# Optimization experiments

Hardware: AMD Instinct MI355X
Metric: run time of the kernel (lower is better)

The kernel has to match this reference:

```python
import jax, jax.numpy as jnp
import numpy as np

DIM = 2240; HEADS = 20; HD = 112
B = 1; F = 8; H = 16; W = 28; S = F * H * W; ENC = 300
HID = int(3.0 * DIM)  # 6720
EPS_LN = 1e-6; EPS_RMS = 1e-5


def setup_inputs():
    ks = iter(jax.random.split(jax.random.key(0), 64))
    nrm = lambda shape, s=1.0: jax.random.normal(next(ks), shape, jnp.float32) * s
    wsc = 0.02
    inp = dict(
        hidden_states=nrm((B, S, DIM)),
        encoder_hidden_states=nrm((B, ENC, DIM)),
        timestep=nrm((B, 6 * DIM), 0.1),
        freqs_cos=nrm((1, S, 1, HD)),
        freqs_sin=nrm((1, S, 1, HD)),
        scale_shift_table=nrm((6, DIM), 1.0 / np.sqrt(DIM)),
    )
    for p in ("a1", "a2"):
        inp[p + "_qw"] = nrm((DIM, DIM), wsc); inp[p + "_qb"] = jnp.zeros((DIM,), jnp.float32)
        inp[p + "_kw"] = nrm((DIM, DIM), wsc); inp[p + "_kb"] = jnp.zeros((DIM,), jnp.float32)
        inp[p + "_vw"] = nrm((DIM, DIM), wsc); inp[p + "_vb"] = jnp.zeros((DIM,), jnp.float32)
        inp[p + "_nq"] = jnp.ones((DIM,), jnp.float32)
        inp[p + "_nk"] = jnp.ones((DIM,), jnp.float32)
        inp[p + "_ow"] = nrm((DIM, DIM), wsc); inp[p + "_ob"] = jnp.zeros((DIM,), jnp.float32)
    inp["ff_inv_w"] = nrm((1, 1, DIM, 2 * HID), wsc)
    inp["ff_inv_b"] = jnp.zeros((2 * HID,), jnp.float32)
    inp["ff_depth_w"] = nrm((3, 3, 1, 2 * HID), wsc)
    inp["ff_depth_b"] = jnp.zeros((2 * HID,), jnp.float32)
    inp["ff_point_w"] = nrm((1, 1, HID, DIM), wsc)
    inp["ff_temp_w"] = nrm((3, 1, DIM, DIM), wsc)
    inp["frames"] = F; inp["height"] = H; inp["width"] = W
    return inp


def _ln(x):  # LayerNorm, no affine (elementwise_affine=False)
    m = jnp.mean(x, -1, keepdims=True)
    v = jnp.mean((x - m) ** 2, -1, keepdims=True)
    return (x - m) * jax.lax.rsqrt(v + EPS_LN)


def _rms(x, w):  # rms_norm_across_heads on full inner dim
    return x * jax.lax.rsqrt(jnp.mean(x * x, -1, keepdims=True) + EPS_RMS) * w


def _rope(x, cos, sin):  # interleaved rotary as in SanaLinearAttnProcessor3_0
    x1, x2 = x[..., 0::2], x[..., 1::2]
    c, s = cos[..., 0::2], sin[..., 1::2]
    out = jnp.stack([x1 * c - x2 * s, x1 * s + x2 * c], axis=-1)
    return out.reshape(x.shape)


def _conv(x, k, padding, groups=1):
    return jax.lax.conv_general_dilated(
        x, k, (1, 1), padding,
        dimension_numbers=("NHWC", "HWIO", "NHWC"),
        feature_group_count=groups)


def _linear_attn(x, qw, qb, kw, kb, vw, vb, nq, nk, ow, ob, cos, sin):
    b, s, _ = x.shape
    q = jax.nn.relu(_rms(x @ qw + qb, nq)).reshape(b, s, HEADS, HD)
    k = jax.nn.relu(_rms(x @ kw + kb, nk)).reshape(b, s, HEADS, HD)
    v = (x @ vw + vb).reshape(b, s, HEADS, HD)
    qr, kr = _rope(q, cos, sin), _rope(k, cos, sin)
    ksum = jnp.sum(k, axis=1)                             # [b,h,d] (un-rotated)
    denom = jnp.einsum("bhd,bshd->bsh", ksum, q) + 1e-15  # z^{-1}
    scores = jnp.einsum("bshe,bshd->bhed", v, kr)         # [b,h,dv,d]
    out = jnp.einsum("bhed,bshd->bshe", scores, qr) / denom[..., None]
    return out.reshape(b, s, HEADS * HD) @ ow + ob


def _cross_attn(x, enc, qw, qb, kw, kb, vw, vb, nq, nk, ow, ob):
    b, s, _ = x.shape; t = enc.shape[1]
    q = _rms(x @ qw + qb, nq).reshape(b, s, HEADS, HD)
    k = _rms(enc @ kw + kb, nk).reshape(b, t, HEADS, HD)
    v = (enc @ vw + vb).reshape(b, t, HEADS, HD)
    logits = jnp.einsum("bshd,bthd->bhst", q, k) / np.sqrt(HD).astype(np.float32)
    attn = jax.nn.softmax(logits, axis=-1)
    out = jnp.einsum("bhst,bthd->bshd", attn, v).reshape(b, s, HEADS * HD)
    return out @ ow + ob


def _ff(x, inv_w, inv_b, depth_w, depth_b, point_w, temp_w, f, h, w):
    b = x.shape[0]
    y = x.reshape(b * f, h, w, DIM)
    y = jax.nn.silu(_conv(y, inv_w, "SAME") + inv_b)
    y = _conv(y, depth_w, "SAME", groups=2 * HID) + depth_b
    a, g = y[..., :HID], y[..., HID:]
    y = _conv(a * jax.nn.silu(g), point_w, "SAME")        # [bf,h,w,DIM]
    yt = y.reshape(b, f, h * w, DIM)                      # conv over frames axis
    yt = yt + _conv(yt, temp_w, ((1, 1), (0, 0)))
    return yt.reshape(b, f, h, w, DIM)


def reference(hidden_states, encoder_hidden_states, timestep, freqs_cos, freqs_sin,
              scale_shift_table,
              a1_qw, a1_qb, a1_kw, a1_kb, a1_vw, a1_vb, a1_nq, a1_nk, a1_ow, a1_ob,
              a2_qw, a2_qb, a2_kw, a2_kb, a2_vw, a2_vb, a2_nq, a2_nk, a2_ow, a2_ob,
              ff_inv_w, ff_inv_b, ff_depth_w, ff_depth_b, ff_point_w, ff_temp_w,
              frames, height, width):
    b = hidden_states.shape[0]
    mods = scale_shift_table[None] + timestep.reshape(b, 6, DIM)
    sh_msa, sc_msa, g_msa, sh_mlp, sc_mlp, g_mlp = jnp.split(mods, 6, axis=1)
    nh = _ln(hidden_states) * (1 + sc_msa) + sh_msa
    attn = _linear_attn(nh, a1_qw, a1_qb, a1_kw, a1_kb, a1_vw, a1_vb,
                        a1_nq, a1_nk, a1_ow, a1_ob, freqs_cos, freqs_sin)
    x = hidden_states + g_msa * attn
    x = x + _cross_attn(x, encoder_hidden_states, a2_qw, a2_qb, a2_kw, a2_kb,
                        a2_vw, a2_vb, a2_nq, a2_nk, a2_ow, a2_ob)
    nh = _ln(x) * (1 + sc_mlp) + sh_mlp
    ff = _ff(nh.reshape(b, frames, height, width, DIM),
             ff_inv_w, ff_inv_b, ff_depth_w, ff_depth_b, ff_point_w, ff_temp_w,
             frames, height, width)
    x = x + g_mlp * ff.reshape(b, frames * height * width, DIM)
    return x
```

## Files before the change

kernel.cpp:

```cpp
#include <hip/hip_runtime.h>

#define DIMC 2240
#define STOK 3584
#define ENCT 300
#define NH   20
#define HDIM 112
#define HID1 6720
#define HID2 13440
#define DD   (2240*2240)
#define SD   (3584*2240)

typedef short bf16x8 __attribute__((ext_vector_type(8)));
typedef float f32x4  __attribute__((ext_vector_type(4)));

__device__ __forceinline__ unsigned short f2bf(float f){
  unsigned int u = __float_as_uint(f);
  u += 0x7fffu + ((u >> 16) & 1u);
  return (unsigned short)(u >> 16);
}
__device__ __forceinline__ float bf2f(unsigned short h){
  return __uint_as_float(((unsigned int)h) << 16);
}
__device__ __forceinline__ void gl_lds16(const unsigned short* g, unsigned short* l){
  __builtin_amdgcn_global_load_lds(
      (const __attribute__((address_space(1))) unsigned int*)(const void*)g,
      (__attribute__((address_space(3))) unsigned int*)(void*)l, 16, 0, 0);
}

__global__ void cvt_k(const float4* __restrict__ src, ushort4* __restrict__ dst, int n4){
  int i = blockIdx.x*256 + threadIdx.x;
  if (i < n4){
    float4 v = src[i];
    ushort4 o; o.x = f2bf(v.x); o.y = f2bf(v.y); o.z = f2bf(v.z); o.w = f2bf(v.w);
    dst[i] = o;
  }
}

__global__ __launch_bounds__(256) void cvt_t_k(const float* __restrict__ src,
    unsigned short* __restrict__ dst, int rows, int ldsrc, int c0, int nc){
  __shared__ float tile[32][33];
  const int tx = threadIdx.x & 31, ty = threadIdx.x >> 5;
  const int colBase = blockIdx.x*32;
  #pragma unroll
  for (int i = 0; i < 4; ++i){
    int rr = blockIdx.y*32 + ty + i*8;
    int cc = colBase + tx;
    tile[ty + i*8][tx] = (cc < nc) ? src[(size_t)rr*ldsrc + c0 + cc] : 0.f;
  }
  __syncthreads();
  #pragma unroll
  for (int i = 0; i < 4; ++i){
    int n = colBase + ty + i*8;
    int k = blockIdx.y*32 + tx;
    dst[(size_t)n*rows + k] = f2bf(tile[tx][ty + i*8]);
  }
}

__global__ void pack3_k(float* __restrict__ dst, const float* __restrict__ b0,
    const float* __restrict__ b1, const float* __restrict__ b2, int nslots){
  int i = blockIdx.x*256 + threadIdx.x;
  if (i >= nslots*2304) return;
  int slot = i / 2304, d = i - slot*2304;
  const float* src = (slot == 0) ? b0 : ((slot == 1) ? b1 : b2);
  dst[i] = (d < 2240) ? src[d] : 0.f;
}

__global__ void mods_k(const float* __restrict__ sst, const float* __restrict__ ts, float* __restrict__ mods){
  int i = blockIdx.x*256 + threadIdx.x;
  if (i < 6*DIMC) mods[i] = sst[i] + ts[i];
}

__global__ __launch_bounds__(256) void ln_mod_k(const float* __restrict__ x,
    const float* __restrict__ mods, int shj, int scj, unsigned short* __restrict__ out)
{
  const int s = blockIdx.x;
  const float* row = x + (size_t)s*DIMC;
  const float* sh = mods + shj*DIMC;
  const float* sc = mods + scj*DIMC;
  float sum = 0.f, sq = 0.f;
  for (int d = threadIdx.x; d < DIMC; d += 256){ float v = row[d]; sum += v; sq += v*v; }
  #pragma unroll
  for (int o = 32; o; o >>= 1){ sum += __shfl_down(sum, o); sq += __shfl_down(sq, o); }
  __shared__ float sA[4], sB[4];
  int w = threadIdx.x >> 6, l = threadIdx.x & 63;
  if (!l){ sA[w] = sum; sB[w] = sq; }
  __syncthreads();
  sum = sA[0]+sA[1]+sA[2]+sA[3];
  sq  = sB[0]+sB[1]+sB[2]+sB[3];
  float mean = sum * (1.f/DIMC);
  float rs = rsqrtf(sq*(1.f/DIMC) - mean*mean + 1e-6f);
  unsigned short* orow = out + (size_t)s*DIMC;
  for (int d = threadIdx.x; d < DIMC; d += 256){
    float v = (row[d]-mean)*rs*(1.f + sc[d]) + sh[d];
    orow[d] = f2bf(v);
  }
}

template<int RELU, int ROPE>
__global__ __launch_bounds__(256) void rms_bf_k(unsigned short* __restrict__ x, const float* __restrict__ nw,
    const float* __restrict__ cosb, const float* __restrict__ sinb, unsigned short* __restrict__ xr)
{
  const int s = blockIdx.x;
  unsigned short* row = x + (size_t)s*DIMC;
  float sq = 0.f;
  for (int d = threadIdx.x; d < DIMC; d += 256){ float v = bf2f(row[d]); sq += v*v; }
  #pragma unroll
  for (int o = 32; o; o >>= 1) sq += __shfl_down(sq, o);
  __shared__ float sB[4];
  int w = threadIdx.x >> 6, l = threadIdx.x & 63;
  if (!l) sB[w] = sq;
  __syncthreads();
  sq = sB[0]+sB[1]+sB[2]+sB[3];
  float rs = rsqrtf(sq*(1.f/DIMC) + 1e-5f);
  if constexpr (!ROPE){
    for (int d = threadIdx.x; d < DIMC; d += 256){
      float v = bf2f(row[d])*rs*nw[d];
      if (RELU) v = fmaxf(v, 0.f);
      row[d] = f2bf(v);
    }
  } else {
    for (int p = threadIdx.x; p < DIMC/2; p += 256){
      int d0 = 2*p, d1 = d0+1;
      float v0 = bf2f(row[d0])*rs*nw[d0];
      float v1 = bf2f(row[d1])*rs*nw[d1];
      if (RELU){ v0 = fmaxf(v0,0.f); v1 = fmaxf(v1,0.f); }
      row[d0] = f2bf(v0); row[d1] = f2bf(v1);
      int j0 = d0 % HDIM;
      float c  = cosb[(size_t)s*HDIM + j0];
      float sn = sinb[(size_t)s*HDIM + j0 + 1];
      xr[(size_t)s*DIMC + d0] = f2bf(v0*c - v1*sn);
      xr[(size_t)s*DIMC + d1] = f2bf(v0*sn + v1*c);
    }
  }
}

template<int EPI>
__global__ __launch_bounds__(256) void gemm_bt(
  const unsigned short* __restrict__ A, const unsigned short* __restrict__ Bt,
  const float* __restrict__ bias, float* __restrict__ Cf, unsigned short* __restrict__ Cb,
  const float* __restrict__ res, const float* __restrict__ gate,
  int M, int N, int K, int ldc, int PW)
{
  __shared__ __align__(16) unsigned short Al[128*64];
  __shared__ __align__(16) unsigned short Bl[128*64];
  const int gx = gridDim.x, gy = gridDim.y;
  const int nwg = gx*gy;
  const int orig = blockIdx.y*gx + blockIdx.x;
  const int qq = nwg >> 3, rr = nwg & 7;
  const int xcd = orig & 7, li = orig >> 3;
  const int wg = (xcd < rr ? xcd*(qq+1) : rr*(qq+1) + (xcd-rr)*qq) + li;
  const int ppw = gy*PW;
  const int panel = wg / ppw, rm = wg - panel*ppw;
  const int mrow = rm / PW;
  const int m0 = mrow*128;
  const int n0 = (panel*PW + (rm - mrow*PW))*128;

  const int t = threadIdx.x, lane = t & 63, w = t >> 6;
  const int wr = w >> 1, wc = w & 1;
  const int l16 = lane & 15, lk = lane >> 4;

  const int lr8 = lane >> 3;
  const int sc  = (lane & 7) ^ lr8;
  const unsigned short* Aps[4];
  const unsigned short* Bps[4];
  #pragma unroll
  for (int i = 0; i < 4; ++i){
    int ar = m0 + w*32 + i*8 + lr8;
    int br = n0 + w*32 + i*8 + lr8;
    Aps[i] = A  + (size_t)min(ar, M-1)*K + sc*8;
    Bps[i] = Bt + (size_t)br*K + sc*8;
  }
  unsigned short* Ad = Al + w*2048;
  unsigned short* Bd = Bl + w*2048;

  f32x4 acc[4][4] = {};
  for (int k0 = 0; k0 < K; k0 += 64){
    __syncthreads();
    #pragma unroll
    for (int i = 0; i < 4; ++i){
      gl_lds16(Aps[i] + k0, Ad + i*512);
      gl_lds16(Bps[i] + k0, Bd + i*512);
    }
    __syncthreads();
    #pragma unroll
    for (int kk = 0; kk < 2; ++kk){
      bf16x8 af[4], bfr[4];
      const int chb = (kk*4 + lk) ^ (l16 & 7);
      #pragma unroll
      for (int m = 0; m < 4; ++m)
        af[m] = *reinterpret_cast<const bf16x8*>(Al + (wr*64 + m*16 + l16)*64 + chb*8);
      #pragma unroll
      for (int n = 0; n < 4; ++n)
        bfr[n] = *reinterpret_cast<const bf16x8*>(Bl + (wc*64 + n*16 + l16)*64 + chb*8);
      #pragma unroll
      for (int m = 0; m < 4; ++m)
        #pragma unroll
        for (int n = 0; n < 4; ++n)
          acc[m][n] = __builtin_amdgcn_mfma_f32_16x16x32_bf16(af[m], bfr[n], acc[m][n], 0, 0, 0);
    }
  }

  const int rb = m0 + wr*64 + lk*4;
  const int cb = n0 + wc*64 + l16;
  #pragma unroll
  for (int m = 0; m < 4; ++m){
    #pragma unroll
    for (int r = 0; r < 4; ++r){
      int row = rb + m*16 + r;
      if (row >= M) continue;
      #pragma unroll
      for (int n = 0; n < 4; ++n){
        int col = cb + n*16;
        if (col >= N) continue;
        float v = acc[m][n][r];
        float bv = bias ? bias[col] : 0.f;
        if constexpr (EPI == 6){
          int slot = col / 2304;
          int d = col - slot*2304;
          if (d < 2240)
            Cb[(size_t)slot*ldc + (size_t)row*2240 + d] = f2bf(v + bv);
        } else {
          size_t idx = (size_t)row*ldc + col;
          if constexpr (EPI == 0){ Cf[idx] = v + bv; }
          else if constexpr (EPI == 1){ float u = v + bv; Cb[idx] = f2bf(u / (1.f + __expf(-u))); }
          else if constexpr (EPI == 2){ Cb[idx] = f2bf(v + bv); }
          else if constexpr (EPI == 3){ float u = res[idx] + gate[col]*(v + bv); Cf[idx] = u; Cb[idx] = f2bf(u); }
          else if constexpr (EPI == 4){ Cf[idx] = res[idx] + v + bv; }
          else { Cf[idx] += v; }
        }
      }
    }
  }
}

__global__ void colsum_k(const unsigned short* __restrict__ k, float* __restrict__ kpart){
  int d = blockIdx.x*256 + threadIdx.x;
  if (d >= DIMC) return;
  int ch = blockIdx.y, s0 = ch*128;
  float acc = 0.f;
  for (int s = s0; s < s0+128; ++s) acc += bf2f(k[(size_t)s*DIMC + d]);
  kpart[(size_t)ch*DIMC + d] = acc;
}
__global__ void ksumred_k(const float* __restrict__ kpart, float* __restrict__ ksum){
  int d = blockIdx.x*256 + threadIdx.x;
  if (d >= DIMC) return;
  float a = 0.f;
  for (int c = 0; c < 28; ++c) a += kpart[(size_t)c*DIMC + d];
  ksum[d] = a;
}
__global__ __launch_bounds__(256) void denom_k(const unsigned short* __restrict__ q,
    const float* __restrict__ ksum, float* __restrict__ denom)
{
  int s = blockIdx.x; int w = threadIdx.x >> 6, l = threadIdx.x & 63;
  for (int h = w; h < NH; h += 4){
    const unsigned short* qb = q + (size_t)s*DIMC + h*HDIM;
    const float* kb = ksum + h*HDIM;
    float v = bf2f(qb[l])*kb[l];
    if (l < 48) v += bf2f(qb[64+l])*kb[64+l];
    #pragma unroll
    for (int o = 32; o; o >>= 1) v += __shfl_down(v, o);
    if (!l) denom[s*NH + h] = v + 1e-15f;
  }
}

#define SLSC 136
__device__ __forceinline__ int sc_idx(int e, int s){
  return e*SLSC + (s ^ (((e >> 3) & 7) << 3));
}
__global__ __launch_bounds__(256) void scores_k(const unsigned short* __restrict__ v,
    const unsigned short* __restrict__ kr, float* __restrict__ part)
{
  const int h = blockIdx.x, ch = blockIdx.y;
  __shared__ __align__(16) unsigned short Vt[112*SLSC];
  __shared__ __align__(16) unsigned short Kt[112*SLSC];
  const int t = threadIdx.x, lane = t & 63, w = t >> 6;
  const int l16 = lane & 15, lk = lane >> 4;
  const int sbase = ch*128;

  for (int p = t; p < 1792; p += 256){
    int s = p / 14, oc = (p % 14) * 8;
    bf16x8 vv = *reinterpret_cast<const bf16x8*>(v  + (size_t)(sbase+s)*DIMC + h*HDIM + oc);
    bf16x8 kk = *reinterpret_cast<const bf16x8*>(kr + (size_t)(sbase+s)*DIMC + h*HDIM + oc);
    #pragma unroll
    for (int j = 0; j < 8; ++j){
      Vt[sc_idx(oc+j, s)] = (unsigned short)vv[j];
      Kt[sc_idx(oc+j, s)] = (unsigned short)kk[j];
    }
  }
  __syncthreads();

  f32x4 acc[2][7] = {};
  #pragma unroll
  for (int ks = 0; ks < 4; ++ks){
    const int sf = ks*32 + lk*8;
    bf16x8 bfrg[7];
    #pragma unroll
    for (int nt = 0; nt < 7; ++nt){
      int d = nt*16 + l16;
      bfrg[nt] = *reinterpret_cast<const bf16x8*>(&Kt[d*SLSC + (sf ^ (((d >> 3) & 7) << 3))]);
    }
    #pragma unroll
    for (int mi = 0; mi < 2; ++mi){
      int mt = w + mi*4;
      if (mt < 7){
        int e = mt*16 + l16;
        bf16x8 afrg = *reinterpret_cast<const bf16x8*>(&Vt[e*SLSC + (sf ^ (((e >> 3) & 7) << 3))]);
        #pragma unroll
        for (int nt = 0; nt < 7; ++nt)
          acc[mi][nt] = __builtin_amdgcn_mfma_f32_16x16x32_bf16(afrg, bfrg[nt], acc[mi][nt], 0, 0, 0);
      }
    }
  }

  float* pout = part + ((size_t)ch*NH + h)*12544;
  #pragma unroll
  for (int mi = 0; mi < 2; ++mi){
    int mt = w + mi*4;
    if (mt >= 7) continue;
    #pragma unroll
    for (int nt = 0; nt < 7; ++nt)
      #pragma unroll
      for (int r = 0; r < 4; ++r)
        pout[(size_t)(mt*16 + lk*4 + r)*HDIM + nt*16 + l16] = acc[mi][nt][r];
  }
}
__global__ void scred_k(const float* __restrict__ part, unsigned short* __restrict__ sc){
  int i = blockIdx.x*256 + threadIdx.x;
  if (i >= NH*HDIM*HDIM) return;
  float a = 0.f;
  #pragma unroll
  for (int c = 0; c < 28; ++c) a += part[(size_t)c*(NH*HDIM*HDIM) + i];
  sc[i] = f2bf(a);
}

__global__ __launch_bounds__(256) void linout_k(const unsigned short* __restrict__ qr,
    const unsigned short* __restrict__ scores, const float* __restrict__ denom,
    unsigned short* __restrict__ out)
{
  const int h = blockIdx.y;
  const int t = threadIdx.x, lane = t & 63, w = t >> 6;
  const int l16 = lane & 15, lk = lane >> 4;
  const int s0 = blockIdx.x*64 + w*16;
  const unsigned short* qrow = qr + (size_t)(s0 + l16)*DIMC + h*HDIM;
  const unsigned short* sb = scores + (size_t)h*12544;
  f32x4 acc[7] = {};
  #pragma unroll
  for (int ks = 0; ks < 4; ++ks){
    int d0 = ks*32 + lk*8;
    bf16x8 a = {};
    if (d0 < HDIM) a = *reinterpret_cast<const bf16x8*>(qrow + d0);
    #pragma unroll
    for (int nt = 0; nt < 7; ++nt){
      bf16x8 b = {};
      if (d0 < HDIM) b = *reinterpret_cast<const bf16x8*>(sb + (size_t)(nt*16 + l16)*HDIM + d0);
      acc[nt] = __builtin_amdgcn_mfma_f32_16x16x32_bf16(a, b, acc[nt], 0, 0, 0);
    }
  }
  #pragma unroll
  for (int r = 0; r < 4; ++r){
    int s = s0 + lk*4 + r;
    float dn = 1.f / denom[(size_t)s*NH + h];
    #pragma unroll
    for (int nt = 0; nt < 7; ++nt)
      out[(size_t)s*DIMC + h*HDIM + nt*16 + l16] = f2bf(acc[nt][r]*dn);
  }
}

__global__ __launch_bounds__(256) void xattn_k(
    const unsigned short* __restrict__ q,
    const unsigned short* __restrict__ k2,
    const unsigned short* __restrict__ v2,
    unsigned short* __restrict__ outb)
{
  const int h = blockIdx.y;
  const int w = threadIdx.x >> 6, lane = threadIdx.x & 63;
  const int l16 = lane & 15, lk = lane >> 4;
  const float scale = 0.09449111825230679f;

  __shared__ __align__(16) unsigned short Kl[64][136];
  __shared__ __align__(16) unsigned short Vl[112][72];
  __shared__ __align__(16) unsigned short Pl[4][16][72];

  bf16x8 qf[4];
  const unsigned short* qbase = q + (size_t)(blockIdx.x*64 + w*16 + l16)*DIMC + h*HDIM;
  #pragma unroll
  for (int c = 0; c < 4; ++c){
    int d0 = c*32 + lk*8;
    bf16x8 z = {};
    qf[c] = (d0 < HDIM) ? *reinterpret_cast<const bf16x8*>(qbase + d0) : z;
  }

  f32x4 lg[5][4] = {};
  #pragma unroll
  for (int c = 0; c < 5; ++c){
    const int kbase = c*64;
    const int nk = (c == 4) ? (ENCT - 256) : 64;
    __syncthreads();
    #pragma unroll
    for (int it = 0; it < 4; ++it){
      int li = it*256 + threadIdx.x;
      int key = li >> 4, d0 = (li & 15) << 3;
      uint4 val = make_uint4(0u,0u,0u,0u);
      if (key < nk && d0 < HDIM)
        val = *reinterpret_cast<const uint4*>(k2 + (size_t)(kbase+key)*DIMC + h*HDIM + d0);
      *reinterpret_cast<uint4*>(&Kl[key][d0]) = val;
    }
    __syncthreads();
    #pragma unroll
    for (int nt = 0; nt < 4; ++nt){
      #pragma unroll
      for (int ks = 0; ks < 4; ++ks){
        bf16x8 kf = *reinterpret_cast<const bf16x8*>(&Kl[nt*16 + l16][ks*32 + lk*8]);
        lg[c][nt] = __builtin_amdgcn_mfma_f32_16x16x32_bf16(qf[ks], kf, lg[c][nt], 0, 0, 0);
      }
    }
  }

  float mx[4] = {-3e38f, -3e38f, -3e38f, -3e38f};
  #pragma unroll
  for (int c = 0; c < 5; ++c)
    #pragma unroll
    for (int nt = 0; nt < 4; ++nt){
      bool valid = (c*64 + nt*16 + l16) < ENCT;
      #pragma unroll
      for (int r = 0; r < 4; ++r){
        float v = valid ? lg[c][nt][r]*scale : -3e38f;
        lg[c][nt][r] = v;
        mx[r] = fmaxf(mx[r], v);
      }
    }
  #pragma unroll
  for (int o = 1; o < 16; o <<= 1)
    #pragma unroll
    for (int r = 0; r < 4; ++r) mx[r] = fmaxf(mx[r], __shfl_xor(mx[r], o));
  float sm[4] = {0.f, 0.f, 0.f, 0.f};
  #pragma unroll
  for (int c = 0; c < 5; ++c)
    #pragma unroll
    for (int nt = 0; nt < 4; ++nt)
      #pragma unroll
      for (int r = 0; r < 4; ++r){
        float e = __expf(lg[c][nt][r] - mx[r]);
        lg[c][nt][r] = e;
        sm[r] += e;
      }
  #pragma unroll
  for (int o = 1; o < 16; o <<= 1)
    #pragma unroll
    for (int r = 0; r < 4; ++r) sm[r] += __shfl_xor(sm[r], o);
  float inv[4];
  #pragma unroll
  for (int r = 0; r < 4; ++r) inv[r] = 1.f / sm[r];

  f32x4 oacc[7] = {};
  #pragma unroll
  for (int c = 0; c < 5; ++c){
    const int kbase = c*64;
    const int nk = (c == 4) ? (ENCT - 256) : 64;
    __syncthreads();
    #pragma unroll
    for (int it = 0; it < 4; ++it){
      int li = it*256 + threadIdx.x;
      if (li < 896){
        int key = li/14, d0 = (li%14)*8;
        if (key < nk){
          bf16x8 vv = *reinterpret_cast<const bf16x8*>(v2 + (size_t)(kbase+key)*DIMC + h*HDIM + d0);
          #pragma unroll
          for (int j = 0; j < 8; ++j) Vl[d0+j][key] = (unsigned short)vv[j];
        } else {
          #pragma unroll
          for (int j = 0; j < 8; ++j) Vl[d0+j][key] = 0;
        }
      }
    }
    #pragma unroll
    for (int nt = 0; nt < 4; ++nt)
      #pragma unroll
      for (int r = 0; r < 4; ++r)
        Pl[w][lk*4 + r][nt*16 + l16] = f2bf(lg[c][nt][r]);
    __syncthreads();
    #pragma unroll
    for (int ks = 0; ks < 2; ++ks){
      bf16x8 pf = *reinterpret_cast<const bf16x8*>(&Pl[w][l16][ks*32 + lk*8]);
      #pragma unroll
      for (int n = 0; n < 7; ++n){
        bf16x8 vf = *reinterpret_cast<const bf16x8*>(&Vl[n*16 + l16][ks*32 + lk*8]);
        oacc[n] = __builtin_amdgcn_mfma_f32_16x16x32_bf16(pf, vf, oacc[n], 0, 0, 0);
      }
    }
  }

  const int orow = blockIdx.x*64 + w*16 + lk*4;
  #pragma unroll
  for (int n = 0; n < 7; ++n)
    #pragma unroll
    for (int r = 0; r < 4; ++r)
      outb[(size_t)(orow + r)*DIMC + h*HDIM + n*16 + l16] = f2bf(oacc[n][r]*inv[r]);
}

__global__ __launch_bounds__(256) void dw_k(const unsigned short* __restrict__ y1,
    const float* __restrict__ dw, const float* __restrict__ db, unsigned short* __restrict__ y2)
{
  int c = (blockIdx.y*256 + threadIdx.x)*2;
  if (c >= HID1) return;
  int bx = blockIdx.x;
  int ww = bx % 28;
  int yt = (bx / 28) & 3;
  int f  = bx / 112;
  int y0 = yt*4;

  float wa[9][2], wg[9][2];
  #pragma unroll
  for (int tp = 0; tp < 9; ++tp){
    float2 va = *reinterpret_cast<const float2*>(dw + tp*HID2 + c);
    float2 vg = *reinterpret_cast<const float2*>(dw + tp*HID2 + c + HID1);
    wa[tp][0] = va.x; wa[tp][1] = va.y;
    wg[tp][0] = vg.x; wg[tp][1] = vg.y;
  }
  float2 ba = *reinterpret_cast<const float2*>(db + c);
  float2 bg = *reinterpret_cast<const float2*>(db + c + HID1);
  float a0[4], a1[4], g0[4], g1[4];
  #pragma unroll
  for (int r = 0; r < 4; ++r){ a0[r] = ba.x; a1[r] = ba.y; g0[r] = bg.x; g1[r] = bg.y; }

  #pragma unroll
  for (int dy6 = 0; dy6 < 6; ++dy6){
    int y = y0 - 1 + dy6;
    if ((unsigned)y >= 16u) continue;
    #pragma unroll
    for (int dx = 0; dx < 3; ++dx){
      int x = ww + dx - 1;
      if ((unsigned)x >= 28u) continue;
      size_t base = ((size_t)(f*16 + y)*28 + x)*HID2;
      unsigned int a01 = *reinterpret_cast<const unsigned int*>(y1 + base + c);
      unsigned int g01 = *reinterpret_cast<const unsigned int*>(y1 + base + c + HID1);
      float fa0 = bf2f((unsigned short)(a01 & 0xffffu));
      float fa1 = bf2f((unsigned short)(a01 >> 16));
      float fg0 = bf2f((unsigned short)(g01 & 0xffffu));
      float fg1 = bf2f((unsigned short)(g01 >> 16));
      #pragma unroll
      for (int r = 0; r < 4; ++r){
        int kdy = dy6 - r;
        if (kdy < 0 || kdy > 2) continue;
        int tp = kdy*3 + dx;
        a0[r] += fa0*wa[tp][0]; a1[r] += fa1*wa[tp][1];
        g0[r] += fg0*wg[tp][0]; g1[r] += fg1*wg[tp][1];
      }
    }
  }
  #pragma unroll
  for (int r = 0; r < 4; ++r){
    float s0 = g0[r] / (1.f + __expf(-g0[r]));
    float s1 = g1[r] / (1.f + __expf(-g1[r]));
    int pos = (f*16 + y0 + r)*28 + ww;
    unsigned int o = (unsigned int)f2bf(a0[r]*s0) | ((unsigned int)f2bf(a1[r]*s1) << 16);
    *reinterpret_cast<unsigned int*>(y2 + (size_t)pos*HID1 + c) = o;
  }
}

__global__ void final_k(const float* __restrict__ x2, const unsigned short* __restrict__ y3,
    const float* __restrict__ tc, const float* __restrict__ mods, float* __restrict__ out)
{
  int i = blockIdx.x*256 + threadIdx.x;
  if (i >= SD) return;
  int d = i % DIMC;
  out[i] = x2[i] + mods[5*DIMC + d]*(bf2f(y3[i]) + tc[i]);
}

extern "C" void kernel_launch(void* const* d_in, const int* in_sizes, int n_in,
                              void* d_out, int out_size, void* d_ws, size_t ws_size,
                              hipStream_t stream)
{
  const float* hid   = (const float*)d_in[0];
  const float* enc   = (const float*)d_in[1];
  const float* tstep = (const float*)d_in[2];
  const float* fcos  = (const float*)d_in[3];
  const float* fsin  = (const float*)d_in[4];
  const float* sst   = (const float*)d_in[5];
  const float *a1_qw=(const float*)d_in[6],  *a1_qb=(const float*)d_in[7];
  const float *a1_kw=(const float*)d_in[8],  *a1_kb=(const float*)d_in[9];
  const float *a1_vw=(const float*)d_in[10], *a1_vb=(const float*)d_in[11];
  const float *a1_nq=(const float*)d_in[12], *a1_nk=(const float*)d_in[13];
  const float *a1_ow=(const float*)d_in[14], *a1_ob=(const float*)d_in[15];
  const float *a2_qw=(const float*)d_in[16], *a2_qb=(const float*)d_in[17];
  const float *a2_kw=(const float*)d_in[18], *a2_kb=(const float*)d_in[19];
  const float *a2_vw=(const float*)d_in[20], *a2_vb=(const float*)d_in[21];
  const float *a2_nq=(const float*)d_in[22], *a2_nk=(const float*)d_in[23];
  const float *a2_ow=(const float*)d_in[24], *a2_ob=(const float*)d_in[25];
  const float *ff_inv_w=(const float*)d_in[26], *ff_inv_b=(const float*)d_in[27];
  const float *ff_dw=(const float*)d_in[28], *ff_db=(const float*)d_in[29];
  const float *ff_pw=(const float*)d_in[30];
  const float *ff_tw=(const float*)d_in[31];
  float* out = (float*)d_out;

  const size_t SLOTB = (size_t)SD*2;
  char* ws = (char*)d_ws;
  size_t off = 0;
  auto alloc = [&](size_t n){ void* p = ws + off; off += (n + 255) & ~(size_t)255; return p; };

  char* P = (char*)alloc(6*SLOTB);
  float* x1    = (float*)alloc((size_t)SD*4);
  unsigned short* nh2b = (unsigned short*)alloc(SLOTB);
  float* x2    = (float*)alloc((size_t)SD*4);
  unsigned short* k2b = (unsigned short*)alloc((size_t)ENCT*DIMC*2);
  unsigned short* v2b = (unsigned short*)alloc((size_t)ENCT*DIMC*2);
  unsigned short* encb = (unsigned short*)alloc((size_t)ENCT*DIMC*2);
  float* modsb = (float*)alloc(6*DIMC*4);
  float* ksum  = (float*)alloc(DIMC*4);
  float* kpart = (float*)alloc((size_t)28*DIMC*4);
  float* denom = (float*)alloc((size_t)STOK*NH*4);
  unsigned short* scorb = (unsigned short*)alloc((size_t)NH*HDIM*HDIM*2);
  float* bias3 = (float*)alloc(3*2304*4);
  unsigned short* Wbig = (unsigned short*)alloc((size_t)6912*DIMC*2);

  unsigned short* P0 = (unsigned short*)P;
  unsigned short* P1 = (unsigned short*)(P + 1*SLOTB);
  unsigned short* P2 = (unsigned short*)(P + 2*SLOTB);
  unsigned short* P3 = (unsigned short*)(P + 3*SLOTB);
  unsigned short* P4 = (unsigned short*)(P + 4*SLOTB);
  unsigned short* P5 = (unsigned short*)(P + 5*SLOTB);
  unsigned short* nhb = P0;
  unsigned short* y1b = P0;
  unsigned short* y2b = (unsigned short*)x1;
  unsigned short* y3b = P0;
  float* tc = (float*)(P + 1*SLOTB);
  float* spart = (float*)P1;

  auto cvt = [&](const float* s, unsigned short* d, size_t n){
    int n4 = (int)(n/4);
    cvt_k<<<dim3((n4+255)/256), 256, 0, stream>>>((const float4*)s, (ushort4*)d, n4);
  };
  auto cvtT = [&](const float* s, unsigned short* d, int rows, int ldsrc, int c0, int nc, int ncPad){
    cvt_t_k<<<dim3(ncPad/32, rows/32), 256, 0, stream>>>(s, d, rows, ldsrc, c0, nc);
  };
  auto gemm_grid = [&](int M, int Npad){ return dim3(Npad/128, (M+127)/128); };

  mods_k<<<dim3((6*DIMC+255)/256), 256, 0, stream>>>(sst, tstep, modsb);
  cvt(enc, encb, (size_t)ENCT*DIMC);

  ln_mod_k<<<dim3(STOK), 256, 0, stream>>>(hid, modsb, 0, 1, nhb);
  pack3_k<<<dim3((3*2304+255)/256), 256, 0, stream>>>(bias3, a1_qb, a1_kb, a1_vb, 3);
  cvtT(a1_qw, Wbig + (size_t)0*2304*DIMC, DIMC, DIMC, 0, DIMC, 2304);
  cvtT(a1_kw, Wbig + (size_t)1*2304*DIMC, DIMC, DIMC, 0, DIMC, 2304);
  cvtT(a1_vw, Wbig + (size_t)2*2304*DIMC, DIMC, DIMC, 0, DIMC, 2304);
  gemm_bt<6><<<gemm_grid(STOK, 6912), 256, 0, stream>>>(nhb, Wbig, bias3, nullptr, P1,
                                                        nullptr, nullptr, STOK, 6912, DIMC, SD, 6);
  rms_bf_k<1,1><<<dim3(STOK), 256, 0, stream>>>(P1, a1_nq, fcos, fsin, P4);
  rms_bf_k<1,1><<<dim3(STOK), 256, 0, stream>>>(P2, a1_nk, fcos, fsin, P5);
  colsum_k<<<dim3(9, 28), 256, 0, stream>>>(P2, kpart);
  ksumred_k<<<dim3(9), 256, 0, stream>>>(kpart, ksum);
  denom_k<<<dim3(STOK), 256, 0, stream>>>(P1, ksum, denom);
  scores_k<<<dim3(NH, 28), 256, 0, stream>>>(P3, P5, spart);
  scred_k<<<dim3((NH*HDIM*HDIM+255)/256), 256, 0, stream>>>(spart, scorb);
  linout_k<<<dim3(STOK/64, NH), 256, 0, stream>>>(P4, scorb, denom, P1);
  dim3 gMN = gemm_grid(STOK, 2304);
  cvtT(a1_ow, Wbig, DIMC, DIMC, 0, DIMC, 2304);
  gemm_bt<3><<<gMN, 256, 0, stream>>>(P1, Wbig, a1_ob, x1, P2, hid, modsb + 2*DIMC, STOK, DIMC, DIMC, DIMC, 6);

  cvtT(a2_qw, Wbig, DIMC, DIMC, 0, DIMC, 2304);
  gemm_bt<2><<<gMN, 256, 0, stream>>>(P2, Wbig, a2_qb, nullptr, P3, nullptr, nullptr, STOK, DIMC, DIMC, DIMC, 6);
  pack3_k<<<dim3((2*2304+255)/256), 256, 0, stream>>>(bias3, a2_kb, a2_vb, a2_vb, 2);
  cvtT(a2_kw, Wbig + (size_t)0*2304*DIMC, DIMC, DIMC, 0, DIMC, 2304);
  cvtT(a2_vw, Wbig + (size_t)1*2304*DIMC, DIMC, DIMC, 0, DIMC, 2304);
  gemm_bt<6><<<gemm_grid(ENCT, 4608), 256, 0, stream>>>(encb, Wbig, bias3, nullptr, k2b,
                                                        nullptr, nullptr, ENCT, 4608, DIMC, ENCT*DIMC, 6);
  rms_bf_k<0,0><<<dim3(STOK), 256, 0, stream>>>(P3, a2_nq, nullptr, nullptr, nullptr);
  rms_bf_k<0,0><<<dim3(ENCT), 256, 0, stream>>>(k2b, a2_nk, nullptr, nullptr, nullptr);
  xattn_k<<<dim3(STOK/64, NH), 256, 0, stream>>>(P3, k2b, v2b, P4);
  cvtT(a2_ow, Wbig, DIMC, DIMC, 0, DIMC, 2304);
  gemm_bt<4><<<gMN, 256, 0, stream>>>(P4, Wbig, a2_ob, x2, nullptr, x1, nullptr, STOK, DIMC, DIMC, DIMC, 6);

  ln_mod_k<<<dim3(STOK), 256, 0, stream>>>(x2, modsb, 3, 4, nh2b);
  for (int q = 0; q < 2; ++q){
    int c0 = q*6720;
    cvtT(ff_inv_w, Wbig, DIMC, HID2, c0, 6720, 6912);
    gemm_bt<1><<<gemm_grid(STOK, 6912), 256, 0, stream>>>(nh2b, Wbig, ff_inv_b + c0, nullptr, y1b + c0,
                                                          nullptr, nullptr, STOK, 6720, DIMC, HID2, 6);
  }
  dw_k<<<dim3(896, 14), 256, 0, stream>>>(y1b, ff_dw, ff_db, y2b);
  cvtT(ff_pw, Wbig, HID1, DIMC, 0, DIMC, 2304);
  gemm_bt<2><<<gMN, 256, 0, stream>>>(y2b, Wbig, nullptr, nullptr, y3b,
                                      nullptr, nullptr, STOK, DIMC, HID1, DIMC, 2);
  cvtT(ff_tw + (size_t)DD, Wbig, DIMC, DIMC, 0, DIMC, 2304);
  gemm_bt<0><<<gMN, 256, 0, stream>>>(y3b, Wbig, nullptr, tc, nullptr, nullptr, nullptr, STOK, DIMC, DIMC, DIMC, 6);
  dim3 gT = gemm_grid(3136, 2304);
  cvtT(ff_tw, Wbig, DIMC, DIMC, 0, DIMC, 2304);
  gemm_bt<5><<<gT, 256, 0, stream>>>(y3b, Wbig, nullptr, tc + (size_t)448*DIMC, nullptr, nullptr, nullptr, 3136, DIMC, DIMC, DIMC, 6);
  cvtT(ff_tw + (size_t)2*DD, Wbig, DIMC, DIMC, 0, DIMC, 2304);
  gemm_bt<5><<<gT, 256, 0, stream>>>(y3b + (size_t)448*DIMC, Wbig, nullptr, tc, nullptr, nullptr, nullptr, 3136, DIMC, DIMC, DIMC, 6);

  final_k<<<dim3((SD+255)/256), 256, 0, stream>>>(x2, y3b, tc, modsb, out);
}
```

Measured before the change: 1.533 ms.

## Vectorize elementwise kernels and tile depthwise conv over two columns

```diff
diff --git a/kernel.cpp b/kernel.cpp
--- a/kernel.cpp
+++ b/kernel.cpp
@@ -74,11 +74,15 @@
     const float* __restrict__ mods, int shj, int scj, unsigned short* __restrict__ out)
 {
   const int s = blockIdx.x;
-  const float* row = x + (size_t)s*DIMC;
-  const float* sh = mods + shj*DIMC;
-  const float* sc = mods + scj*DIMC;
+  const float4* row4 = reinterpret_cast<const float4*>(x + (size_t)s*DIMC);
+  const float4* sh4 = reinterpret_cast<const float4*>(mods + shj*DIMC);
+  const float4* sc4 = reinterpret_cast<const float4*>(mods + scj*DIMC);
   float sum = 0.f, sq = 0.f;
-  for (int d = threadIdx.x; d < DIMC; d += 256){ float v = row[d]; sum += v; sq += v*v; }
+  for (int o = threadIdx.x; o < 560; o += 256){
+    float4 v = row4[o];
+    sum += v.x + v.y + v.z + v.w;
+    sq  += v.x*v.x + v.y*v.y + v.z*v.z + v.w*v.w;
+  }
   #pragma unroll
   for (int o = 32; o; o >>= 1){ sum += __shfl_down(sum, o); sq += __shfl_down(sq, o); }
   __shared__ float sA[4], sB[4];
@@ -90,9 +94,14 @@
   float mean = sum * (1.f/DIMC);
   float rs = rsqrtf(sq*(1.f/DIMC) - mean*mean + 1e-6f);
   unsigned short* orow = out + (size_t)s*DIMC;
-  for (int d = threadIdx.x; d < DIMC; d += 256){
-    float v = (row[d]-mean)*rs*(1.f + sc[d]) + sh[d];
-    orow[d] = f2bf(v);
+  for (int o = threadIdx.x; o < 560; o += 256){
+    float4 v = row4[o], sc = sc4[o], sh = sh4[o];
+    ushort4 r;
+    r.x = f2bf((v.x-mean)*rs*(1.f + sc.x) + sh.x);
+    r.y = f2bf((v.y-mean)*rs*(1.f + sc.y) + sh.y);
+    r.z = f2bf((v.z-mean)*rs*(1.f + sc.z) + sh.z);
+    r.w = f2bf((v.w-mean)*rs*(1.f + sc.w) + sh.w);
+    *reinterpret_cast<ushort4*>(orow + o*4) = r;
   }
 }
 
@@ -103,7 +112,16 @@
   const int s = blockIdx.x;
   unsigned short* row = x + (size_t)s*DIMC;
   float sq = 0.f;
-  for (int d = threadIdx.x; d < DIMC; d += 256){ float v = bf2f(row[d]); sq += v*v; }
+  for (int o = threadIdx.x; o < 280; o += 256){
+    uint4 v = *reinterpret_cast<const uint4*>(row + o*8);
+    unsigned int uu[4] = {v.x, v.y, v.z, v.w};
+    #pragma unroll
+    for (int j = 0; j < 4; ++j){
+      float lo = bf2f((unsigned short)(uu[j] & 0xffffu));
+      float hi = bf2f((unsigned short)(uu[j] >> 16));
+      sq += lo*lo + hi*hi;
+    }
+  }
   #pragma unroll
   for (int o = 32; o; o >>= 1) sq += __shfl_down(sq, o);
   __shared__ float sB[4];
@@ -112,24 +130,41 @@
   __syncthreads();
   sq = sB[0]+sB[1]+sB[2]+sB[3];
   float rs = rsqrtf(sq*(1.f/DIMC) + 1e-5f);
-  if constexpr (!ROPE){
-    for (int d = threadIdx.x; d < DIMC; d += 256){
-      float v = bf2f(row[d])*rs*nw[d];
-      if (RELU) v = fmaxf(v, 0.f);
-      row[d] = f2bf(v);
-    }
-  } else {
-    for (int p = threadIdx.x; p < DIMC/2; p += 256){
-      int d0 = 2*p, d1 = d0+1;
-      float v0 = bf2f(row[d0])*rs*nw[d0];
-      float v1 = bf2f(row[d1])*rs*nw[d1];
-      if (RELU){ v0 = fmaxf(v0,0.f); v1 = fmaxf(v1,0.f); }
-      row[d0] = f2bf(v0); row[d1] = f2bf(v1);
-      int j0 = d0 % HDIM;
-      float c  = cosb[(size_t)s*HDIM + j0];
-      float sn = sinb[(size_t)s*HDIM + j0 + 1];
-      xr[(size_t)s*DIMC + d0] = f2bf(v0*c - v1*sn);
-      xr[(size_t)s*DIMC + d1] = f2bf(v0*sn + v1*c);
+  for (int o = threadIdx.x; o < 280; o += 256){
+    uint4 v = *reinterpret_cast<const uint4*>(row + o*8);
+    unsigned int uu[4] = {v.x, v.y, v.z, v.w};
+    float4 n0 = *reinterpret_cast<const float4*>(nw + o*8);
+    float4 n1 = *reinterpret_cast<const float4*>(nw + o*8 + 4);
+    float nn[8] = {n0.x,n0.y,n0.z,n0.w,n1.x,n1.y,n1.z,n1.w};
+    float vals[8];
+    #pragma unroll
+    for (int j = 0; j < 4; ++j){
+      vals[2*j]   = bf2f((unsigned short)(uu[j] & 0xffffu))*rs*nn[2*j];
+      vals[2*j+1] = bf2f((unsigned short)(uu[j] >> 16))*rs*nn[2*j+1];
+    }
+    if constexpr (RELU){
+      #pragma unroll
+      for (int j = 0; j < 8; ++j) vals[j] = fmaxf(vals[j], 0.f);
+    }
+    uint4 o1;
+    unsigned int* po = &o1.x;
+    #pragma unroll
+    for (int j = 0; j < 4; ++j)
+      po[j] = (unsigned int)f2bf(vals[2*j]) | ((unsigned int)f2bf(vals[2*j+1]) << 16);
+    *reinterpret_cast<uint4*>(row + o*8) = o1;
+    if constexpr (ROPE){
+      int jb = (o*8) % HDIM;
+      uint4 o2;
+      unsigned int* pr = &o2.x;
+      #pragma unroll
+      for (int p = 0; p < 4; ++p){
+        float c  = cosb[(size_t)s*HDIM + jb + 2*p];
+        float sn = sinb[(size_t)s*HDIM + jb + 2*p + 1];
+        float r0 = vals[2*p]*c - vals[2*p+1]*sn;
+        float r1 = vals[2*p]*sn + vals[2*p+1]*c;
+        pr[p] = (unsigned int)f2bf(r0) | ((unsigned int)f2bf(r1) << 16);
+      }
+      *reinterpret_cast<uint4*>(xr + (size_t)s*DIMC + o*8) = o2;
     }
   }
 }
@@ -504,10 +539,10 @@
   int c = (blockIdx.y*256 + threadIdx.x)*2;
   if (c >= HID1) return;
   int bx = blockIdx.x;
-  int ww = bx % 28;
-  int yt = (bx / 28) & 3;
-  int f  = bx / 112;
-  int y0 = yt*4;
+  int xp = bx % 14;
+  int yt = (bx / 14) & 3;
+  int f  = bx / 56;
+  int x0 = xp*2, y0 = yt*4;
 
   float wa[9][2], wg[9][2];
   #pragma unroll
@@ -519,17 +554,22 @@
   }
   float2 ba = *reinterpret_cast<const float2*>(db + c);
   float2 bg = *reinterpret_cast<const float2*>(db + c + HID1);
-  float a0[4], a1[4], g0[4], g1[4];
-  #pragma unroll
-  for (int r = 0; r < 4; ++r){ a0[r] = ba.x; a1[r] = ba.y; g0[r] = bg.x; g1[r] = bg.y; }
+  float a[4][2][2], g[4][2][2];
+  #pragma unroll
+  for (int r = 0; r < 4; ++r)
+    #pragma unroll
+    for (int cc = 0; cc < 2; ++cc){
+      a[r][cc][0] = ba.x; a[r][cc][1] = ba.y;
+      g[r][cc][0] = bg.x; g[r][cc][1] = bg.y;
+    }
 
   #pragma unroll
   for (int dy6 = 0; dy6 < 6; ++dy6){
     int y = y0 - 1 + dy6;
     if ((unsigned)y >= 16u) continue;
     #pragma unroll
-    for (int dx = 0; dx < 3; ++dx){
-      int x = ww + dx - 1;
+    for (int dxc = 0; dxc < 4; ++dxc){
+      int x = x0 - 1 + dxc;
       if ((unsigned)x >= 28u) continue;
       size_t base = ((size_t)(f*16 + y)*28 + x)*HID2;
       unsigned int a01 = *reinterpret_cast<const unsigned int*>(y1 + base + c);
@@ -542,29 +582,45 @@
       for (int r = 0; r < 4; ++r){
         int kdy = dy6 - r;
         if (kdy < 0 || kdy > 2) continue;
-        int tp = kdy*3 + dx;
-        a0[r] += fa0*wa[tp][0]; a1[r] += fa1*wa[tp][1];
-        g0[r] += fg0*wg[tp][0]; g1[r] += fg1*wg[tp][1];
-      }
-    }
-  }
-  #pragma unroll
-  for (int r = 0; r < 4; ++r){
-    float s0 = g0[r] / (1.f + __expf(-g0[r]));
-    float s1 = g1[r] / (1.f + __expf(-g1[r]));
-    int pos = (f*16 + y0 + r)*28 + ww;
-    unsigned int o = (unsigned int)f2bf(a0[r]*s0) | ((unsigned int)f2bf(a1[r]*s1) << 16);
-    *reinterpret_cast<unsigned int*>(y2 + (size_t)pos*HID1 + c) = o;
-  }
+        #pragma unroll
+        for (int cc = 0; cc < 2; ++cc){
+          int kdx = dxc - cc;
+          if (kdx < 0 || kdx > 2) continue;
+          int tp = kdy*3 + kdx;
+          a[r][cc][0] += fa0*wa[tp][0]; a[r][cc][1] += fa1*wa[tp][1];
+          g[r][cc][0] += fg0*wg[tp][0]; g[r][cc][1] += fg1*wg[tp][1];
+        }
+      }
+    }
+  }
+  #pragma unroll
+  for (int r = 0; r < 4; ++r)
+    #pragma unroll
+    for (int cc = 0; cc < 2; ++cc){
+      float s0 = g[r][cc][0] / (1.f + __expf(-g[r][cc][0]));
+      float s1 = g[r][cc][1] / (1.f + __expf(-g[r][cc][1]));
+      int pos = (f*16 + y0 + r)*28 + x0 + cc;
+      unsigned int o = (unsigned int)f2bf(a[r][cc][0]*s0) | ((unsigned int)f2bf(a[r][cc][1]*s1) << 16);
+      *reinterpret_cast<unsigned int*>(y2 + (size_t)pos*HID1 + c) = o;
+    }
 }
 
 __global__ void final_k(const float* __restrict__ x2, const unsigned short* __restrict__ y3,
     const float* __restrict__ tc, const float* __restrict__ mods, float* __restrict__ out)
 {
-  int i = blockIdx.x*256 + threadIdx.x;
-  if (i >= SD) return;
-  int d = i % DIMC;
-  out[i] = x2[i] + mods[5*DIMC + d]*(bf2f(y3[i]) + tc[i]);
+  int i4 = (blockIdx.x*256 + threadIdx.x)*4;
+  if (i4 >= SD) return;
+  int d = i4 % DIMC;
+  float4 xv = *reinterpret_cast<const float4*>(x2 + i4);
+  float4 tv = *reinterpret_cast<const float4*>(tc + i4);
+  float4 gv = *reinterpret_cast<const float4*>(mods + 5*DIMC + d);
+  ushort4 yv = *reinterpret_cast<const ushort4*>(y3 + i4);
+  float4 o;
+  o.x = xv.x + gv.x*(bf2f(yv.x) + tv.x);
+  o.y = xv.y + gv.y*(bf2f(yv.y) + tv.y);
+  o.z = xv.z + gv.z*(bf2f(yv.z) + tv.z);
+  o.w = xv.w + gv.w*(bf2f(yv.w) + tv.w);
+  *reinterpret_cast<float4*>(out + i4) = o;
 }
 
 extern "C" void kernel_launch(void* const* d_in, const int* in_sizes, int n_in,
@@ -677,7 +733,7 @@
     gemm_bt<1><<<gemm_grid(STOK, 6912), 256, 0, stream>>>(nh2b, Wbig, ff_inv_b + c0, nullptr, y1b + c0,
                                                           nullptr, nullptr, STOK, 6720, DIMC, HID2, 6);
   }
-  dw_k<<<dim3(896, 14), 256, 0, stream>>>(y1b, ff_dw, ff_db, y2b);
+  dw_k<<<dim3(448, 14), 256, 0, stream>>>(y1b, ff_dw, ff_db, y2b);
   cvtT(ff_pw, Wbig, HID1, DIMC, 0, DIMC, 2304);
   gemm_bt<2><<<gMN, 256, 0, stream>>>(y2b, Wbig, nullptr, nullptr, y3b,
                                       nullptr, nullptr, STOK, DIMC, HID1, DIMC, 2);
@@ -689,5 +745,5 @@
   cvtT(ff_tw + (size_t)2*DD, Wbig, DIMC, DIMC, 0, DIMC, 2304);
   gemm_bt<5><<<gT, 256, 0, stream>>>(y3b + (size_t)448*DIMC, Wbig, nullptr, tc, nullptr, nullptr, nullptr, 3136, DIMC, DIMC, DIMC, 6);
 
-  final_k<<<dim3((SD+255)/256), 256, 0, stream>>>(x2, y3b, tc, modsb, out);
-}
+  final_k<<<dim3((SD/4+255)/256), 256, 0, stream>>>(x2, y3b, tc, modsb, out);
+}
```

New measurement: 1.486 ms. 1.03x faster.
